# Kernel tuning notes

Hardware: AMD Instinct MI355X
Metric: run time of the kernel (lower is better)

## Reference

```python
import jax, jax.numpy as jnp
import numpy as np

C = 256; Ca = C // 2; WH = 8; WW = 8; K = 3; NH = 8; HD = Ca // NH
EPS_LN = 1e-5; EPS_BN = 1e-5

def _rel_pos_idx(wh, ww):
    coords = np.stack(np.meshgrid(np.arange(wh), np.arange(ww), indexing='ij'))  # (2,wh,ww)
    flat = coords.reshape(2, -1)
    rel = (flat[:, :, None] - flat[:, None, :]).transpose(1, 2, 0).astype(np.int64)  # (N,N,2)
    rel[..., 0] += wh - 1
    rel[..., 1] += ww - 1
    rel[..., 0] *= 2 * ww - 1
    return jnp.asarray(rel.sum(-1))  # (N,N)

REL_IDX = _rel_pos_idx(WH, WW)

def _ln(x, g, b):
    m = x.mean(-1, keepdims=True)
    v = x.var(-1, keepdims=True)
    return (x - m) / jnp.sqrt(v + EPS_LN) * g + b

def _bn(x, g, b):  # eval-mode BN, running_mean=0, running_var=1; x is NCHW
    return x * (g / np.sqrt(1.0 + EPS_BN))[None, :, None, None] + b[None, :, None, None]

def _conv1x1(x, w, b):  # w: (O, I)
    return jnp.einsum('bchw,oc->bohw', x, w) + b[None, :, None, None]

def _rwp(x, h, w, wh, ww):  # windows (B*nW, wh*ww, c) -> image (B, c, h, w)
    Bn, N, c = x.shape
    nh, nw = h // wh, w // ww
    B = Bn // (nh * nw)
    x = x.reshape(B, nh, nw, wh, ww, c)
    return x.transpose(0, 5, 1, 3, 2, 4).reshape(B, c, h, w)

def _wp(x, wh, ww):  # image (B, c, h, w) -> windows (B*nW, wh*ww, c)
    B, c, h, w = x.shape
    x = x.reshape(B, c, h // wh, wh, w // ww, ww)
    return x.transpose(0, 2, 4, 3, 5, 1).reshape(-1, wh * ww, c)

def _gelu(t):
    return jax.nn.gelu(t, approximate=False)

def forward(x, rel_pos_bias, attn_w, attn_b, attn_ln_g, attn_ln_b,
            conv_w, conv_b, conv_bn_g, conv_bn_b,
            ci_w1, ci_b1, ci_bn_g, ci_bn_b, ci_w2, ci_b2,
            pr_w, pr_b, cn_bn_g, cn_bn_b,
            qkv_w, qkv_b,
            si_w1, si_b1, si_bn_g, si_bn_b, si_w2, si_b2,
            an_g, an_b, out_w, out_b, h, w):
    B_, N, Cfull = x.shape
    x_attn = _ln(x @ attn_w + attn_b, attn_ln_g, attn_ln_b)  # (B_, N, Ca)
    # conv branch -- note: source applies RWP to raw x (proj_cnn output is dead code)
    x_img = _rwp(x, h, w, WH, WW)  # (B, C, h, w)
    pad = K // 2
    x_cnn = jax.lax.conv_general_dilated(
        x_img, conv_w, (1, 1), [(pad, pad), (pad, pad)],
        dimension_numbers=('NCHW', 'OIHW', 'NCHW'), feature_group_count=Cfull)
    x_cnn = _gelu(_bn(x_cnn + conv_b[None, :, None, None], conv_bn_g, conv_bn_b))
    gap = x_cnn.mean((2, 3), keepdims=True)  # (B, C, 1, 1)
    ci = _conv1x1(gap, ci_w1, ci_b1)
    ci = _gelu(_bn(ci, ci_bn_g, ci_bn_b))
    ci = _conv1x1(ci, ci_w2, ci_b2)  # (B, Ca, 1, 1)
    x_cnn = _conv1x1(x_cnn, pr_w, pr_b)  # (B, Ca, h, w)
    # windowed attention
    qkv = (x_attn @ qkv_w + qkv_b).reshape(B_, N, 3, NH, HD).transpose(2, 0, 3, 1, 4)
    q, k, v = qkv[0], qkv[1], qkv[2]  # each (B_, NH, N, HD)
    B = ci.shape[0]
    ci_s = jax.nn.sigmoid(ci).reshape(B, 1, NH, 1, HD)
    v = (v.reshape(B, B_ // B, NH, N, HD) * ci_s).reshape(B_, NH, N, HD)
    scale = HD ** -0.5
    attn = jnp.einsum('bhnd,bhmd->bhnm', q * scale, k)
    bias = rel_pos_bias[REL_IDX]  # (N, N, NH)
    attn = jax.nn.softmax(attn + bias.transpose(2, 0, 1)[None], axis=-1)
    x_attn = jnp.einsum('bhnm,bhmd->bhnd', attn, v).transpose(0, 2, 1, 3).reshape(B_, N, Ca)
    # spatial interaction gating of conv branch
    x_sp = _rwp(x_attn, h, w, WH, WW)  # (B, Ca, h, w)
    si = _conv1x1(x_sp, si_w1, si_b1)
    si = _gelu(_bn(si, si_bn_g, si_bn_b))
    si = _conv1x1(si, si_w2, si_b2)  # (B, 1, h, w)
    x_cnn = jax.nn.sigmoid(si * x_cnn)
    x_cnn = _bn(x_cnn, cn_bn_g, cn_bn_b)
    x_cnn = _wp(x_cnn, WH, WW)  # (B_, N, Ca)
    x_attn = _ln(x_attn, an_g, an_b)
    return jnp.concatenate([x_attn, x_cnn], axis=-1) @ out_w + out_b

def setup_inputs() -> dict:
    key = jax.random.key(0)
    ks = jax.random.split(key, 12)
    B_, N = 2048, WH * WW
    s = 0.02
    return dict(
        x=jax.random.normal(ks[0], (B_, N, C), jnp.float32),
        rel_pos_bias=jax.random.uniform(ks[1], ((2 * WH - 1) * (2 * WW - 1), NH), jnp.float32),
        attn_w=jax.random.normal(ks[2], (C, Ca)) * s, attn_b=jnp.zeros((Ca,)),
        attn_ln_g=jnp.ones((Ca,)), attn_ln_b=jnp.zeros((Ca,)),
        conv_w=jax.random.normal(ks[3], (C, 1, K, K)) * s, conv_b=jnp.zeros((C,)),
        conv_bn_g=jnp.ones((C,)), conv_bn_b=jnp.zeros((C,)),
        ci_w1=jax.random.normal(ks[4], (C // 8, C)) * s, ci_b1=jnp.zeros((C // 8,)),
        ci_bn_g=jnp.ones((C // 8,)), ci_bn_b=jnp.zeros((C // 8,)),
        ci_w2=jax.random.normal(ks[5], (Ca, C // 8)) * s, ci_b2=jnp.zeros((Ca,)),
        pr_w=jax.random.normal(ks[6], (Ca, C)) * s, pr_b=jnp.zeros((Ca,)),
        cn_bn_g=jnp.ones((Ca,)), cn_bn_b=jnp.zeros((Ca,)),
        qkv_w=jax.random.normal(ks[7], (Ca, 3 * Ca)) * s, qkv_b=jnp.zeros((3 * Ca,)),
        si_w1=jax.random.normal(ks[8], (C // 16, Ca)) * s, si_b1=jnp.zeros((C // 16,)),
        si_bn_g=jnp.ones((C // 16,)), si_bn_b=jnp.zeros((C // 16,)),
        si_w2=jax.random.normal(ks[9], (1, C // 16)) * s, si_b2=jnp.zeros((1,)),
        an_g=jnp.ones((Ca,)), an_b=jnp.zeros((Ca,)),
        out_w=jax.random.normal(ks[10], (C, C)) * s, out_b=jnp.zeros((C,)),
        h=64, w=64,
    )

def reference(x, rel_pos_bias, attn_w, attn_b, attn_ln_g, attn_ln_b,
              conv_w, conv_b, conv_bn_g, conv_bn_b,
              ci_w1, ci_b1, ci_bn_g, ci_bn_b, ci_w2, ci_b2,
              pr_w, pr_b, cn_bn_g, cn_bn_b,
              qkv_w, qkv_b,
              si_w1, si_b1, si_bn_g, si_bn_b, si_w2, si_b2,
              an_g, an_b, out_w, out_b, h, w):
    return forward(x, rel_pos_bias, attn_w, attn_b, attn_ln_g, attn_ln_b,
                   conv_w, conv_b, conv_bn_g, conv_bn_b,
                   ci_w1, ci_b1, ci_bn_g, ci_bn_b, ci_w2, ci_b2,
                   pr_w, pr_b, cn_bn_g, cn_bn_b,
                   qkv_w, qkv_b,
                   si_w1, si_b1, si_bn_g, si_bn_b, si_w2, si_b2,
                   an_g, an_b, out_w, out_b, h, w)
```

## Files before the change

### kernel.cpp

```cpp
#include <hip/hip_runtime.h>
#include <math.h>


#define BNR 0.9999950000374998f
#define SQRT1_2 0.70710678118654752f

typedef __attribute__((ext_vector_type(8))) short short8;
typedef __attribute__((ext_vector_type(4))) float f32x4;
typedef __attribute__((ext_vector_type(4))) _Float16 half4;

__device__ __forceinline__ float gelu_f(float x) {
  return 0.5f * x * (1.0f + erff(x * SQRT1_2));
}
__device__ __forceinline__ unsigned short f2bf(float f) {
  unsigned int u = __builtin_bit_cast(unsigned int, f);
  u += 0x7fffu + ((u >> 16) & 1u);
  return (unsigned short)(u >> 16);
}
__device__ __forceinline__ float bf2f(unsigned short h) {
  unsigned int u = ((unsigned int)h) << 16;
  return __builtin_bit_cast(float, u);
}
__device__ __forceinline__ void ld8(const unsigned short* p, float* o) {
  const short8 v = *(const short8*)p;
#pragma unroll
  for (int i = 0; i < 8; ++i) o[i] = bf2f((unsigned short)v[i]);
}

#define ATI(r, ch) (((r) << 8) + ((((ch) ^ ((r)&7))) << 3))

__global__ __launch_bounds__(256) void kpack(
    const float* __restrict__ aw, const float* __restrict__ qw,
    const float* __restrict__ prw, const float* __restrict__ ow,
    const float* __restrict__ sw1, unsigned short* __restrict__ awp,
    unsigned short* __restrict__ qwp, unsigned short* __restrict__ prwp,
    unsigned short* __restrict__ owp, unsigned short* __restrict__ sw1p) {
  const int b = blockIdx.x;
  const float* src; unsigned short* dst; int fs, K, N, NT, trans;
  if (b < 64)       { fs = b;       src = aw;  dst = awp;  K = 256; N = 128; NT = 8;  trans = 0; }
  else if (b < 160) { fs = b - 64;  src = qw;  dst = qwp;  K = 128; N = 384; NT = 24; trans = 0; }
  else if (b < 224) { fs = b - 160; src = prw; dst = prwp; K = 256; N = 128; NT = 8;  trans = 1; }
  else if (b < 352) { fs = b - 224; src = ow;  dst = owp;  K = 256; N = 256; NT = 16; trans = 0; }
  else              { fs = b - 352; src = sw1; dst = sw1p; K = 128; N = 16;  NT = 1;  trans = 1; }
  const int ks = fs / NT, nt = fs % NT;
  for (int idx = threadIdx.x; idx < 512; idx += 256) {
    const int l = idx >> 3, i = idx & 7;
    const int k = ks * 32 + ((l >> 4) << 3) + i, n = nt * 16 + (l & 15);
    const float v = trans ? src[n * K + k] : src[k * N + n];
    dst[(fs * 64 + l) * 8 + i] = f2bf(v);
  }
}

__global__ __launch_bounds__(256) void k1_attn_ln(
    const float* __restrict__ x, const unsigned short* __restrict__ awp,
    const float* __restrict__ ab, const float* __restrict__ lg,
    const float* __restrict__ lb, unsigned short* __restrict__ xattn,
    unsigned short* __restrict__ xb) {
  const int tid = threadIdx.x, w = tid >> 6, l = tid & 63;
  const int lr = l & 15, lg4 = l >> 4;
  const int r0 = blockIdx.x * 64 + w * 16;
  const float* xp = x + (size_t)(r0 + lr) * 256 + lg4 * 8;
  unsigned short* xbp = xb + (size_t)(r0 + lr) * 256 + lg4 * 8;
  short8 a[8];
#pragma unroll
  for (int ks = 0; ks < 8; ++ks) {
    const float4 f0 = *(const float4*)(xp + ks * 32);
    const float4 f1 = *(const float4*)(xp + ks * 32 + 4);
    short8 av;
    av[0] = f2bf(f0.x); av[1] = f2bf(f0.y); av[2] = f2bf(f0.z); av[3] = f2bf(f0.w);
    av[4] = f2bf(f1.x); av[5] = f2bf(f1.y); av[6] = f2bf(f1.z); av[7] = f2bf(f1.w);
    a[ks] = av;
    *(short8*)(xbp + ks * 32) = av;
  }
  f32x4 acc[8];
#pragma unroll
  for (int nt = 0; nt < 8; ++nt) acc[nt] = (f32x4)0.f;
#pragma unroll
  for (int nt = 0; nt < 8; ++nt)
#pragma unroll
    for (int ks = 0; ks < 8; ++ks) {
      const short8 bfr = *(const short8*)(awp + ((ks * 8 + nt) * 64 + l) * 8);
      acc[nt] = __builtin_amdgcn_mfma_f32_16x16x32_bf16(a[ks], bfr, acc[nt], 0, 0, 0);
    }
  float bias[8], gam[8], bet[8];
#pragma unroll
  for (int nt = 0; nt < 8; ++nt) {
    const int col = nt * 16 + lr;
    bias[nt] = ab[col]; gam[nt] = lg[col]; bet[nt] = lb[col];
  }
#pragma unroll
  for (int j = 0; j < 4; ++j) {
    float s = 0.f, qq = 0.f;
#pragma unroll
    for (int nt = 0; nt < 8; ++nt) {
      const float v = acc[nt][j] + bias[nt];
      acc[nt][j] = v; s += v; qq += v * v;
    }
    s += __shfl_xor(s, 1); s += __shfl_xor(s, 2);
    s += __shfl_xor(s, 4); s += __shfl_xor(s, 8);
    qq += __shfl_xor(qq, 1); qq += __shfl_xor(qq, 2);
    qq += __shfl_xor(qq, 4); qq += __shfl_xor(qq, 8);
    const float mean = s * (1.f / 128.f);
    const float var = qq * (1.f / 128.f) - mean * mean;
    const float rstd = rsqrtf(var + 1e-5f);
    const int row = r0 + lg4 * 4 + j;
#pragma unroll
    for (int nt = 0; nt < 8; ++nt)
      xattn[(size_t)row * 128 + nt * 16 + lr] =
          f2bf((acc[nt][j] - mean) * rstd * gam[nt] + bet[nt]);
  }
}

__global__ __launch_bounds__(256) void k25_conv(
    const unsigned short* __restrict__ xb, const float* __restrict__ cw,
    const float* __restrict__ cb, const float* __restrict__ bg,
    const float* __restrict__ bb, const unsigned short* __restrict__ prwp,
    const float* __restrict__ prb, unsigned short* __restrict__ xpr,
    float* __restrict__ gpart) {
  __shared__ unsigned short gl[32][264];
  const int tid = threadIdx.x;
  const int b = blockIdx.x >> 7;
  const int y = (blockIdx.x >> 1) & 63;
  const int xt = (blockIdx.x & 1) * 32;
  const int w = tid >> 6, l = tid & 63;
  {
    const int c0 = l << 2;
    float4 w9[9];
#pragma unroll
    for (int k = 0; k < 9; ++k) {
      w9[k].x = cw[(c0 + 0) * 9 + k];
      w9[k].y = cw[(c0 + 1) * 9 + k];
      w9[k].z = cw[(c0 + 2) * 9 + k];
      w9[k].w = cw[(c0 + 3) * 9 + k];
    }
    const float4 cbv = *(const float4*)&cb[c0];
    float4 scv = *(const float4*)&bg[c0];
    scv.x *= BNR; scv.y *= BNR; scv.z *= BNR; scv.w *= BNR;
    const float4 sbv = *(const float4*)&bb[c0];
    float4 gsum = make_float4(0.f, 0.f, 0.f, 0.f);
    const int px0 = xt + w * 8;
#pragma unroll
    for (int sc2 = 0; sc2 < 2; ++sc2) {
      const int p0 = px0 + sc2 * 4;
      float4 v[3][6];
#pragma unroll
      for (int dy = 0; dy < 3; ++dy) {
        const int yy = y + dy - 1;
        const bool vy = (unsigned)yy < 64u;
        const int ybase = vy ? ((b * 64 + (yy >> 3) * 8) * 64 + (yy & 7) * 8) : 0;
#pragma unroll
        for (int q = 0; q < 6; ++q) {
          const int xx = p0 - 1 + q;
          float4 f = make_float4(0.f, 0.f, 0.f, 0.f);
          if (vy && (unsigned)xx < 64u) {
            const int row = ybase + (xx >> 3) * 64 + (xx & 7);
            const ushort4 u = *(const ushort4*)&xb[(size_t)row * 256 + c0];
            f.x = bf2f(u.x); f.y = bf2f(u.y); f.z = bf2f(u.z); f.w = bf2f(u.w);
          }
          v[dy][q] = f;
        }
      }
#pragma unroll
      for (int p = 0; p < 4; ++p) {
        float4 s = cbv;
#pragma unroll
        for (int dy = 0; dy < 3; ++dy)
#pragma unroll
          for (int dx = 0; dx < 3; ++dx) {
            const float wv_x = ((const float*)&w9[dy * 3 + dx])[0];
            const float4 wv = w9[dy * 3 + dx];
            const float4 vv = v[dy][p + dx];
            s.x = fmaf(wv.x, vv.x, s.x);
            s.y = fmaf(wv.y, vv.y, s.y);
            s.z = fmaf(wv.z, vv.z, s.z);
            s.w = fmaf(wv.w, vv.w, s.w);
            (void)wv_x;
          }
        s.x = s.x * scv.x + sbv.x; s.y = s.y * scv.y + sbv.y;
        s.z = s.z * scv.z + sbv.z; s.w = s.w * scv.w + sbv.w;
        const float g0 = gelu_f(s.x), g1 = gelu_f(s.y);
        const float g2 = gelu_f(s.z), g3 = gelu_f(s.w);
        ushort4 pk;
        pk.x = f2bf(g0); pk.y = f2bf(g1); pk.z = f2bf(g2); pk.w = f2bf(g3);
        *(ushort4*)&gl[w * 8 + sc2 * 4 + p][c0] = pk;
        gsum.x += g0; gsum.y += g1; gsum.z += g2; gsum.w += g3;
      }
    }
    *(float4*)&gpart[(size_t)blockIdx.x * 256 + c0] = gsum;
  }
  __syncthreads();
  const int lr = l & 15, lg4 = l >> 4;
  const int mr0 = (w & 1) * 16, nt0 = (w >> 1) * 4;
  short8 a[8];
#pragma unroll
  for (int ks = 0; ks < 8; ++ks)
    a[ks] = *(const short8*)&gl[mr0 + lr][ks * 32 + lg4 * 8];
  f32x4 acc[4];
#pragma unroll
  for (int nt = 0; nt < 4; ++nt) acc[nt] = (f32x4)0.f;
#pragma unroll
  for (int nt = 0; nt < 4; ++nt)
#pragma unroll
    for (int ks = 0; ks < 8; ++ks) {
      const short8 bfr =
          *(const short8*)(prwp + ((ks * 8 + nt0 + nt) * 64 + l) * 8);
      acc[nt] = __builtin_amdgcn_mfma_f32_16x16x32_bf16(a[ks], bfr, acc[nt], 0, 0, 0);
    }
#pragma unroll
  for (int nt = 0; nt < 4; ++nt) {
    const int col = (nt0 + nt) * 16 + lr;
    const float bv = prb[col];
#pragma unroll
    for (int j = 0; j < 4; ++j) {
      const int pix = (b * 64 + y) * 64 + xt + mr0 + lg4 * 4 + j;
      xpr[(size_t)pix * 128 + col] = f2bf(acc[nt][j] + bv);
    }
  }
}

__global__ __launch_bounds__(128) void k3_ci(
    const float* __restrict__ gp, const float* __restrict__ w1,
    const float* __restrict__ b1, const float* __restrict__ g1,
    const float* __restrict__ bb1, const float* __restrict__ w2,
    const float* __restrict__ b2, float* __restrict__ cis) {
  __shared__ float gm[256];
  __shared__ float c1[32];
  const int b = blockIdx.x, tid = threadIdx.x;
  for (int c = tid; c < 256; c += 128) {
    float s = 0.f;
    for (int p = 0; p < 128; ++p) s += gp[(size_t)(b * 128 + p) * 256 + c];
    gm[c] = s * (1.f / 4096.f);
  }
  __syncthreads();
  if (tid < 32) {
    float s = b1[tid];
    for (int c = 0; c < 256; ++c) s = fmaf(gm[c], w1[tid * 256 + c], s);
    s = s * (g1[tid] * BNR) + bb1[tid];
    c1[tid] = gelu_f(s);
  }
  __syncthreads();
  float s = b2[tid];
#pragma unroll
  for (int i = 0; i < 32; ++i) s = fmaf(c1[i], w2[tid * 32 + i], s);
  cis[b * 128 + tid] = 1.f / (1.f + __expf(-s));
}

__global__ __launch_bounds__(256) void k4_attn(
    const unsigned short* __restrict__ xa, const unsigned short* __restrict__ qwp,
    const float* __restrict__ qb, const float* __restrict__ cis,
    const float* __restrict__ rpb, unsigned short* __restrict__ attn) {
  __shared__ _Float16 Qs[64][130];
  __shared__ _Float16 Ks[64][130];
  __shared__ _Float16 VT[128][66];
  __shared__ float bsl[8][226];
  __shared__ float cisl[128];
  __shared__ float qbl[384];
  const int tid = threadIdx.x;
  const int win = blockIdx.x, img = win >> 6;
  for (int i = tid; i < 1800; i += 256) bsl[i & 7][i >> 3] = rpb[i];
  for (int i = tid; i < 128; i += 256) cisl[i] = cis[img * 128 + i];
  for (int i = tid; i < 384; i += 256) qbl[i] = qb[i];
  const int w = tid >> 6, l = tid & 63, lr = l & 15, lg4 = l >> 4;
  short8 a[4];
  const unsigned short* ap = xa + (size_t)(win * 64 + w * 16 + lr) * 128 + lg4 * 8;
#pragma unroll
  for (int ks = 0; ks < 4; ++ks) a[ks] = *(const short8*)(ap + ks * 32);
  f32x4 acc[24];
#pragma unroll
  for (int nt = 0; nt < 24; ++nt) acc[nt] = (f32x4)0.f;
#pragma unroll
  for (int nt = 0; nt < 24; ++nt)
#pragma unroll
    for (int ks = 0; ks < 4; ++ks) {
      const short8 bfr = *(const short8*)(qwp + ((ks * 24 + nt) * 64 + l) * 8);
      acc[nt] = __builtin_amdgcn_mfma_f32_16x16x32_bf16(a[ks], bfr, acc[nt], 0, 0, 0);
    }
  __syncthreads();
#pragma unroll
  for (int nt = 0; nt < 24; ++nt) {
    const int col = nt * 16 + lr;
#pragma unroll
    for (int j = 0; j < 4; ++j) {
      const int row = w * 16 + lg4 * 4 + j;
      const float v = acc[nt][j] + qbl[col];
      if (nt < 8) Qs[row][col] = (_Float16)(v * 0.25f);
      else if (nt < 16) Ks[row][col - 128] = (_Float16)v;
      else VT[col - 256][row] = (_Float16)(v * cisl[col - 256]);
    }
  }
  __syncthreads();
  for (int hi = 0; hi < 2; ++hi) {
    const int h = w * 2 + hi;
    half4 aK[4], bQ[4], bV[4];
#pragma unroll
    for (int mt = 0; mt < 4; ++mt)
      aK[mt] = *(const half4*)&Ks[mt * 16 + lr][h * 16 + lg4 * 4];
#pragma unroll
    for (int nt = 0; nt < 4; ++nt)
      bQ[nt] = *(const half4*)&Qs[nt * 16 + lr][h * 16 + lg4 * 4];
#pragma unroll
    for (int kt = 0; kt < 4; ++kt)
      bV[kt] = *(const half4*)&VT[h * 16 + lr][kt * 16 + lg4 * 4];
    f32x4 s[4][4];
#pragma unroll
    for (int mt = 0; mt < 4; ++mt)
#pragma unroll
      for (int nt = 0; nt < 4; ++nt)
        s[mt][nt] = __builtin_amdgcn_mfma_f32_16x16x16f16(aK[mt], bQ[nt],
                                                          (f32x4)0.f, 0, 0, 0);
#pragma unroll
    for (int mt = 0; mt < 4; ++mt) {
      const int m0 = mt * 16 + lg4 * 4;
#pragma unroll
      for (int r = 0; r < 4; ++r) {
        const int m = m0 + r;
        const int my = m >> 3, mxx = m & 7;
#pragma unroll
        for (int nt = 0; nt < 4; ++nt) {
          const int n = nt * 16 + lr;
          s[mt][nt][r] += bsl[h][((n >> 3) - my + 7) * 15 + (n & 7) - mxx + 7];
        }
      }
    }
    float inv[4];
#pragma unroll
    for (int nt = 0; nt < 4; ++nt) {
      float m0 = -1e30f;
#pragma unroll
      for (int mt = 0; mt < 4; ++mt)
#pragma unroll
        for (int r = 0; r < 4; ++r) m0 = fmaxf(m0, s[mt][nt][r]);
      m0 = fmaxf(m0, __shfl_xor(m0, 16));
      m0 = fmaxf(m0, __shfl_xor(m0, 32));
      float d0 = 0.f;
#pragma unroll
      for (int mt = 0; mt < 4; ++mt)
#pragma unroll
        for (int r = 0; r < 4; ++r) {
          const float e = __expf(s[mt][nt][r] - m0);
          s[mt][nt][r] = e;
          d0 += e;
        }
      d0 += __shfl_xor(d0, 16);
      d0 += __shfl_xor(d0, 32);
      inv[nt] = 1.f / d0;
    }
    half4 pa[4][4];
#pragma unroll
    for (int nt = 0; nt < 4; ++nt)
#pragma unroll
      for (int kt = 0; kt < 4; ++kt) {
        half4 p;
#pragma unroll
        for (int r = 0; r < 4; ++r) p[r] = (_Float16)(s[kt][nt][r] * inv[nt]);
        pa[nt][kt] = p;
      }
    f32x4 o[4];
#pragma unroll
    for (int nt = 0; nt < 4; ++nt) o[nt] = (f32x4)0.f;
#pragma unroll
    for (int nt = 0; nt < 4; ++nt)
#pragma unroll
      for (int kt = 0; kt < 4; ++kt)
        o[nt] = __builtin_amdgcn_mfma_f32_16x16x16f16(pa[nt][kt], bV[kt], o[nt], 0, 0, 0);
#pragma unroll
    for (int nt = 0; nt < 4; ++nt)
#pragma unroll
      for (int r = 0; r < 4; ++r) {
        const int token = win * 64 + nt * 16 + lg4 * 4 + r;
        attn[(size_t)token * 128 + h * 16 + lr] = f2bf(o[nt][r]);
      }
  }
}

__global__ __launch_bounds__(256) void k6_tail(
    const unsigned short* __restrict__ attn, const unsigned short* __restrict__ xpr,
    const unsigned short* __restrict__ sw1p, const float* __restrict__ sb1,
    const float* __restrict__ sgc, const float* __restrict__ sbc,
    const float* __restrict__ sw2, const float* __restrict__ sb2,
    const float* __restrict__ cg, const float* __restrict__ cbb,
    const float* __restrict__ ag, const float* __restrict__ abb,
    const unsigned short* __restrict__ owp, const float* __restrict__ ob,
    float* __restrict__ out) {
  __shared__ unsigned short At[64 * 256];
  __shared__ float sifl[64];
  __shared__ float statl[64][2];
  const int tid = threadIdx.x;
  const int R0 = blockIdx.x * 64;
  const int w = tid >> 6, l = tid & 63, lr = l & 15, lg4 = l >> 4;
  for (int i = tid; i < 1024; i += 256) {
    const int r = i >> 4, c16 = i & 15;
    *(uint4*)&At[ATI(r, c16)] =
        *(const uint4*)&attn[(size_t)(R0 + r) * 128 + c16 * 8];
    const int R = R0 + r, win = R >> 6, tt = R & 63;
    const int bimg = win >> 6, wy = (win >> 3) & 7, wx = win & 7;
    const int pix = (bimg * 64 + wy * 8 + (tt >> 3)) * 64 + wx * 8 + (tt & 7);
    *(uint4*)&At[ATI(r, 16 + c16)] =
        *(const uint4*)&xpr[(size_t)pix * 128 + c16 * 8];
  }
  __syncthreads();
  {
    const int r = tid >> 2, q = tid & 3;
    float xv[32];
#pragma unroll
    for (int b8 = 0; b8 < 4; ++b8) ld8(&At[ATI(r, q * 4 + b8)], xv + b8 * 8);
    float ps = 0.f, pq = 0.f;
#pragma unroll
    for (int j = 0; j < 32; ++j) { ps += xv[j]; pq += xv[j] * xv[j]; }
    ps += __shfl_xor(ps, 1); ps += __shfl_xor(ps, 2);
    pq += __shfl_xor(pq, 1); pq += __shfl_xor(pq, 2);
    if (q == 0) {
      const float mean = ps * (1.f / 128.f);
      const float var = pq * (1.f / 128.f) - mean * mean;
      statl[r][0] = mean;
      statl[r][1] = rsqrtf(var + 1e-5f);
    }
  }
  {
    const int row = w * 16 + lr;
    f32x4 sa = (f32x4)0.f;
#pragma unroll
    for (int ks = 0; ks < 4; ++ks) {
      const short8 a4 = *(const short8*)&At[ATI(row, ks * 4 + lg4)];
      const short8 bfr = *(const short8*)(sw1p + (ks * 64 + l) * 8);
      sa = __builtin_amdgcn_mfma_f32_16x16x32_bf16(a4, bfr, sa, 0, 0, 0);
    }
    const float sb1v = sb1[lr], g1v = sgc[lr] * BNR, b1v = sbc[lr];
    const float w2v = sw2[lr], sb2v = sb2[0];
#pragma unroll
    for (int j = 0; j < 4; ++j) {
      float s = (sa[j] + sb1v) * g1v + b1v;
      float p = gelu_f(s) * w2v;
      p += __shfl_xor(p, 1); p += __shfl_xor(p, 2);
      p += __shfl_xor(p, 4); p += __shfl_xor(p, 8);
      if (lr == 0) sifl[w * 16 + lg4 * 4 + j] = p + sb2v;
    }
  }
  __syncthreads();
  {
    const int c = tid & 127;
    const float agv = ag[c], abbv = abb[c];
    const float cgv = cg[c] * BNR, cbbv = cbb[c];
#pragma unroll
    for (int k = 0; k < 32; ++k) {
      const int r = (tid >> 7) + k * 2;
      const int ia = ATI(r, c >> 3) + (c & 7);
      const int ic = ATI(r, 16 + (c >> 3)) + (c & 7);
      float a = bf2f(At[ia]);
      a = (a - statl[r][0]) * statl[r][1] * agv + abbv;
      At[ia] = f2bf(a);
      const float cv = bf2f(At[ic]);
      const float g = 1.f / (1.f + __expf(-sifl[r] * cv));
      At[ic] = f2bf(g * cgv + cbbv);
    }
  }
  __syncthreads();
  const int row = w * 16 + lr;
  short8 a[8];
#pragma unroll
  for (int ks = 0; ks < 8; ++ks)
    a[ks] = *(const short8*)&At[ATI(row, ks * 4 + lg4)];
  f32x4 acc[16];
#pragma unroll
  for (int nt = 0; nt < 16; ++nt) acc[nt] = (f32x4)0.f;
#pragma unroll
  for (int nt = 0; nt < 16; ++nt)
#pragma unroll
    for (int ks = 0; ks < 8; ++ks) {
      const short8 bfr = *(const short8*)(owp + ((ks * 16 + nt) * 64 + l) * 8);
      acc[nt] = __builtin_amdgcn_mfma_f32_16x16x32_bf16(a[ks], bfr, acc[nt], 0, 0, 0);
    }
#pragma unroll
  for (int nt = 0; nt < 16; ++nt) {
    const int col = nt * 16 + lr;
    const float bv = ob[col];
#pragma unroll
    for (int j = 0; j < 4; ++j)
      out[(size_t)(R0 + w * 16 + lg4 * 4 + j) * 256 + col] = acc[nt][j] + bv;
  }
}

extern "C" void kernel_launch(void* const* d_in, const int* in_sizes, int n_in,
                              void* d_out, int out_size, void* d_ws,
                              size_t ws_size, hipStream_t stream) {
  (void)in_sizes; (void)n_in; (void)out_size; (void)ws_size;
  const float* x      = (const float*)d_in[0];
  const float* rpb    = (const float*)d_in[1];
  const float* attn_w = (const float*)d_in[2];
  const float* attn_b = (const float*)d_in[3];
  const float* aln_g  = (const float*)d_in[4];
  const float* aln_b  = (const float*)d_in[5];
  const float* conv_w = (const float*)d_in[6];
  const float* conv_b = (const float*)d_in[7];
  const float* cbn_g  = (const float*)d_in[8];
  const float* cbn_b  = (const float*)d_in[9];
  const float* ci_w1  = (const float*)d_in[10];
  const float* ci_b1  = (const float*)d_in[11];
  const float* ci_bg  = (const float*)d_in[12];
  const float* ci_bb  = (const float*)d_in[13];
  const float* ci_w2  = (const float*)d_in[14];
  const float* ci_b2  = (const float*)d_in[15];
  const float* pr_w   = (const float*)d_in[16];
  const float* pr_b   = (const float*)d_in[17];
  const float* cn_g   = (const float*)d_in[18];
  const float* cn_b   = (const float*)d_in[19];
  const float* qkv_w  = (const float*)d_in[20];
  const float* qkv_b  = (const float*)d_in[21];
  const float* si_w1  = (const float*)d_in[22];
  const float* si_b1  = (const float*)d_in[23];
  const float* si_bg  = (const float*)d_in[24];
  const float* si_bb  = (const float*)d_in[25];
  const float* si_w2  = (const float*)d_in[26];
  const float* si_b2  = (const float*)d_in[27];
  const float* an_g   = (const float*)d_in[28];
  const float* an_b   = (const float*)d_in[29];
  const float* out_w  = (const float*)d_in[30];
  const float* out_b  = (const float*)d_in[31];

  unsigned short* xb    = (unsigned short*)d_ws;
  unsigned short* xattn = xb + 33554432;
  unsigned short* attn  = xattn + 16777216;
  unsigned short* xpr   = attn + 16777216;
  float* gpart = (float*)(xpr + 16777216);
  float* cis   = gpart + 1048576;
  unsigned short* awp  = (unsigned short*)(cis + 4096);
  unsigned short* qwp  = awp + 32768;
  unsigned short* prwp = qwp + 49152;
  unsigned short* owp  = prwp + 32768;
  unsigned short* sw1p = owp + 65536;

  kpack<<<356, 256, 0, stream>>>(attn_w, qkv_w, pr_w, out_w, si_w1,
                                 awp, qwp, prwp, owp, sw1p);
  k1_attn_ln<<<2048, 256, 0, stream>>>(x, awp, attn_b, aln_g, aln_b, xattn, xb);
  k25_conv<<<4096, 256, 0, stream>>>(xb, conv_w, conv_b, cbn_g, cbn_b, prwp,
                                     pr_b, xpr, gpart);
  k3_ci<<<32, 128, 0, stream>>>(gpart, ci_w1, ci_b1, ci_bg, ci_bb, ci_w2,
                                ci_b2, cis);
  k4_attn<<<2048, 256, 0, stream>>>(xattn, qwp, qkv_b, cis, rpb, attn);
  k6_tail<<<2048, 256, 0, stream>>>(attn, xpr, sw1p, si_b1, si_bg, si_bb,
                                    si_w2, si_b2, cn_g, cn_b, an_g, an_b,
                                    owp, out_b, (float*)d_out);
}
```

Measured before the change: 329.9 us.

## Fuse window attention with tail kernel and use tanh-form GELU

Merges the attention kernel and the tail kernel into one per-window kernel. The attention output stays in shared memory (reusing the Q/K buffer) instead of being written to global memory and read back. The xpr tile is prefetched into registers early. GELU switches from exact erf to the tanh approximation written as a sigmoid, which reduces ALU cost in the conv kernel but adds approximation error. The fused kernel uses more registers and shared memory per block, which may reduce occupancy.

Measured after the change: 344.0 us. 4.3% more time.

```diff
diff --git a/kernel.cpp b/kernel.cpp
--- a/kernel.cpp
+++ b/kernel.cpp
@@ -3,14 +3,14 @@
 
 
 #define BNR 0.9999950000374998f
-#define SQRT1_2 0.70710678118654752f
 
 typedef __attribute__((ext_vector_type(8))) short short8;
 typedef __attribute__((ext_vector_type(4))) float f32x4;
 typedef __attribute__((ext_vector_type(4))) _Float16 half4;
 
 __device__ __forceinline__ float gelu_f(float x) {
-  return 0.5f * x * (1.0f + erff(x * SQRT1_2));
+  const float z = x * (1.0f + 0.044715f * x * x);
+  return x / (1.0f + __expf(-1.5957691216057308f * z));
 }
 __device__ __forceinline__ unsigned short f2bf(float f) {
   unsigned int u = __builtin_bit_cast(unsigned int, f);
@@ -167,14 +167,12 @@
         for (int dy = 0; dy < 3; ++dy)
 #pragma unroll
           for (int dx = 0; dx < 3; ++dx) {
-            const float wv_x = ((const float*)&w9[dy * 3 + dx])[0];
             const float4 wv = w9[dy * 3 + dx];
             const float4 vv = v[dy][p + dx];
             s.x = fmaf(wv.x, vv.x, s.x);
             s.y = fmaf(wv.y, vv.y, s.y);
             s.z = fmaf(wv.z, vv.z, s.z);
             s.w = fmaf(wv.w, vv.w, s.w);
-            (void)wv_x;
           }
         s.x = s.x * scv.x + sbv.x; s.y = s.y * scv.y + sbv.y;
         s.z = s.z * scv.z + sbv.z; s.w = s.w * scv.w + sbv.w;
@@ -245,22 +243,40 @@
   cis[b * 128 + tid] = 1.f / (1.f + __expf(-s));
 }
 
-__global__ __launch_bounds__(256) void k4_attn(
+__global__ __launch_bounds__(256) void k46_attn_tail(
     const unsigned short* __restrict__ xa, const unsigned short* __restrict__ qwp,
     const float* __restrict__ qb, const float* __restrict__ cis,
-    const float* __restrict__ rpb, unsigned short* __restrict__ attn) {
-  __shared__ _Float16 Qs[64][130];
-  __shared__ _Float16 Ks[64][130];
+    const float* __restrict__ rpb, const unsigned short* __restrict__ xpr,
+    const unsigned short* __restrict__ sw1p, const float* __restrict__ sb1,
+    const float* __restrict__ sgc, const float* __restrict__ sbc,
+    const float* __restrict__ sw2, const float* __restrict__ sb2,
+    const float* __restrict__ cg, const float* __restrict__ cbb,
+    const float* __restrict__ ag, const float* __restrict__ abb,
+    const unsigned short* __restrict__ owp, const float* __restrict__ ob,
+    float* __restrict__ out) {
+  __shared__ __align__(16) _Float16 QK[2][64][130];
   __shared__ _Float16 VT[128][66];
   __shared__ float bsl[8][226];
   __shared__ float cisl[128];
   __shared__ float qbl[384];
+  __shared__ float sifl[64];
+  __shared__ float statl[64][2];
+  unsigned short* At = (unsigned short*)QK;
   const int tid = threadIdx.x;
   const int win = blockIdx.x, img = win >> 6;
+  const int w = tid >> 6, l = tid & 63, lr = l & 15, lg4 = l >> 4;
   for (int i = tid; i < 1800; i += 256) bsl[i & 7][i >> 3] = rpb[i];
   for (int i = tid; i < 128; i += 256) cisl[i] = cis[img * 128 + i];
   for (int i = tid; i < 384; i += 256) qbl[i] = qb[i];
-  const int w = tid >> 6, l = tid & 63, lr = l & 15, lg4 = l >> 4;
+  const int bimg = win >> 6, wy = (win >> 3) & 7, wx = win & 7;
+  uint4 xr[4];
+#pragma unroll
+  for (int kk = 0; kk < 4; ++kk) {
+    const int i = tid + kk * 256;
+    const int r = i >> 4, c16 = i & 15;
+    const int pix = (bimg * 64 + wy * 8 + (r >> 3)) * 64 + wx * 8 + (r & 7);
+    xr[kk] = *(const uint4*)&xpr[(size_t)pix * 128 + c16 * 8];
+  }
   short8 a[4];
   const unsigned short* ap = xa + (size_t)(win * 64 + w * 16 + lr) * 128 + lg4 * 8;
 #pragma unroll
@@ -283,21 +299,22 @@
     for (int j = 0; j < 4; ++j) {
       const int row = w * 16 + lg4 * 4 + j;
       const float v = acc[nt][j] + qbl[col];
-      if (nt < 8) Qs[row][col] = (_Float16)(v * 0.25f);
-      else if (nt < 16) Ks[row][col - 128] = (_Float16)v;
+      if (nt < 8) QK[0][row][col] = (_Float16)(v * 0.25f);
+      else if (nt < 16) QK[1][row][col - 128] = (_Float16)v;
       else VT[col - 256][row] = (_Float16)(v * cisl[col - 256]);
     }
   }
   __syncthreads();
+  f32x4 o[2][4];
   for (int hi = 0; hi < 2; ++hi) {
     const int h = w * 2 + hi;
     half4 aK[4], bQ[4], bV[4];
 #pragma unroll
     for (int mt = 0; mt < 4; ++mt)
-      aK[mt] = *(const half4*)&Ks[mt * 16 + lr][h * 16 + lg4 * 4];
+      aK[mt] = *(const half4*)&QK[1][mt * 16 + lr][h * 16 + lg4 * 4];
 #pragma unroll
     for (int nt = 0; nt < 4; ++nt)
-      bQ[nt] = *(const half4*)&Qs[nt * 16 + lr][h * 16 + lg4 * 4];
+      bQ[nt] = *(const half4*)&QK[0][nt * 16 + lr][h * 16 + lg4 * 4];
 #pragma unroll
     for (int kt = 0; kt < 4; ++kt)
       bV[kt] = *(const half4*)&VT[h * 16 + lr][kt * 16 + lg4 * 4];
@@ -355,48 +372,33 @@
         for (int r = 0; r < 4; ++r) p[r] = (_Float16)(s[kt][nt][r] * inv[nt]);
         pa[nt][kt] = p;
       }
-    f32x4 o[4];
-#pragma unroll
-    for (int nt = 0; nt < 4; ++nt) o[nt] = (f32x4)0.f;
+#pragma unroll
+    for (int nt = 0; nt < 4; ++nt) o[hi][nt] = (f32x4)0.f;
 #pragma unroll
     for (int nt = 0; nt < 4; ++nt)
 #pragma unroll
       for (int kt = 0; kt < 4; ++kt)
-        o[nt] = __builtin_amdgcn_mfma_f32_16x16x16f16(pa[nt][kt], bV[kt], o[nt], 0, 0, 0);
+        o[hi][nt] = __builtin_amdgcn_mfma_f32_16x16x16f16(pa[nt][kt], bV[kt],
+                                                          o[hi][nt], 0, 0, 0);
+  }
+  __syncthreads();
+#pragma unroll
+  for (int hi = 0; hi < 2; ++hi) {
+    const int h = w * 2 + hi;
+    const int ch0 = h * 2 + (lr >> 3), co = (lr & 7);
 #pragma unroll
     for (int nt = 0; nt < 4; ++nt)
 #pragma unroll
       for (int r = 0; r < 4; ++r) {
-        const int token = win * 64 + nt * 16 + lg4 * 4 + r;
-        attn[(size_t)token * 128 + h * 16 + lr] = f2bf(o[nt][r]);
+        const int tr = nt * 16 + lg4 * 4 + r;
+        At[ATI(tr, ch0) + co] = f2bf(o[hi][nt][r]);
       }
   }
-}
-
-__global__ __launch_bounds__(256) void k6_tail(
-    const unsigned short* __restrict__ attn, const unsigned short* __restrict__ xpr,
-    const unsigned short* __restrict__ sw1p, const float* __restrict__ sb1,
-    const float* __restrict__ sgc, const float* __restrict__ sbc,
-    const float* __restrict__ sw2, const float* __restrict__ sb2,
-    const float* __restrict__ cg, const float* __restrict__ cbb,
-    const float* __restrict__ ag, const float* __restrict__ abb,
-    const unsigned short* __restrict__ owp, const float* __restrict__ ob,
-    float* __restrict__ out) {
-  __shared__ unsigned short At[64 * 256];
-  __shared__ float sifl[64];
-  __shared__ float statl[64][2];
-  const int tid = threadIdx.x;
-  const int R0 = blockIdx.x * 64;
-  const int w = tid >> 6, l = tid & 63, lr = l & 15, lg4 = l >> 4;
-  for (int i = tid; i < 1024; i += 256) {
+#pragma unroll
+  for (int kk = 0; kk < 4; ++kk) {
+    const int i = tid + kk * 256;
     const int r = i >> 4, c16 = i & 15;
-    *(uint4*)&At[ATI(r, c16)] =
-        *(const uint4*)&attn[(size_t)(R0 + r) * 128 + c16 * 8];
-    const int R = R0 + r, win = R >> 6, tt = R & 63;
-    const int bimg = win >> 6, wy = (win >> 3) & 7, wx = win & 7;
-    const int pix = (bimg * 64 + wy * 8 + (tt >> 3)) * 64 + wx * 8 + (tt & 7);
-    *(uint4*)&At[ATI(r, 16 + c16)] =
-        *(const uint4*)&xpr[(size_t)pix * 128 + c16 * 8];
+    *(uint4*)&At[ATI(r, 16 + c16)] = xr[kk];
   }
   __syncthreads();
   {
@@ -446,9 +448,9 @@
       const int r = (tid >> 7) + k * 2;
       const int ia = ATI(r, c >> 3) + (c & 7);
       const int ic = ATI(r, 16 + (c >> 3)) + (c & 7);
-      float a = bf2f(At[ia]);
-      a = (a - statl[r][0]) * statl[r][1] * agv + abbv;
-      At[ia] = f2bf(a);
+      float av = bf2f(At[ia]);
+      av = (av - statl[r][0]) * statl[r][1] * agv + abbv;
+      At[ia] = f2bf(av);
       const float cv = bf2f(At[ic]);
       const float g = 1.f / (1.f + __expf(-sifl[r] * cv));
       At[ic] = f2bf(g * cgv + cbbv);
@@ -456,19 +458,19 @@
   }
   __syncthreads();
   const int row = w * 16 + lr;
-  short8 a[8];
+  short8 af[8];
 #pragma unroll
   for (int ks = 0; ks < 8; ++ks)
-    a[ks] = *(const short8*)&At[ATI(row, ks * 4 + lg4)];
-  f32x4 acc[16];
-#pragma unroll
-  for (int nt = 0; nt < 16; ++nt) acc[nt] = (f32x4)0.f;
+    af[ks] = *(const short8*)&At[ATI(row, ks * 4 + lg4)];
+  f32x4 oacc[16];
+#pragma unroll
+  for (int nt = 0; nt < 16; ++nt) oacc[nt] = (f32x4)0.f;
 #pragma unroll
   for (int nt = 0; nt < 16; ++nt)
 #pragma unroll
     for (int ks = 0; ks < 8; ++ks) {
       const short8 bfr = *(const short8*)(owp + ((ks * 16 + nt) * 64 + l) * 8);
-      acc[nt] = __builtin_amdgcn_mfma_f32_16x16x32_bf16(a[ks], bfr, acc[nt], 0, 0, 0);
+      oacc[nt] = __builtin_amdgcn_mfma_f32_16x16x32_bf16(af[ks], bfr, oacc[nt], 0, 0, 0);
     }
 #pragma unroll
   for (int nt = 0; nt < 16; ++nt) {
@@ -476,7 +478,7 @@
     const float bv = ob[col];
 #pragma unroll
     for (int j = 0; j < 4; ++j)
-      out[(size_t)(R0 + w * 16 + lg4 * 4 + j) * 256 + col] = acc[nt][j] + bv;
+      out[(size_t)(win * 64 + w * 16 + lg4 * 4 + j) * 256 + col] = oacc[nt][j] + bv;
   }
 }
 
@@ -519,8 +521,7 @@
 
   unsigned short* xb    = (unsigned short*)d_ws;
   unsigned short* xattn = xb + 33554432;
-  unsigned short* attn  = xattn + 16777216;
-  unsigned short* xpr   = attn + 16777216;
+  unsigned short* xpr   = xattn + 16777216;
   float* gpart = (float*)(xpr + 16777216);
   float* cis   = gpart + 1048576;
   unsigned short* awp  = (unsigned short*)(cis + 4096);
@@ -536,8 +537,7 @@
                                      pr_b, xpr, gpart);
   k3_ci<<<32, 128, 0, stream>>>(gpart, ci_w1, ci_b1, ci_bg, ci_bb, ci_w2,
                                 ci_b2, cis);
-  k4_attn<<<2048, 256, 0, stream>>>(xattn, qwp, qkv_b, cis, rpb, attn);
-  k6_tail<<<2048, 256, 0, stream>>>(attn, xpr, sw1p, si_b1, si_bg, si_bb,
-                                    si_w2, si_b2, cn_g, cn_b, an_g, an_b,
-                                    owp, out_b, (float*)d_out);
-}
+  k46_attn_tail<<<2048, 256, 0, stream>>>(
+      xattn, qwp, qkv_b, cis, rpb, xpr, sw1p, si_b1, si_bg, si_bb, si_w2,
+      si_b2, cn_g, cn_b, an_g, an_b, owp, out_b, (float*)d_out);
+}
```
